# Kernel optimization log

Hardware: AMD Instinct MI355X
Metric: run time of the kernel (lower is better)

The kernel has to match this reference:

```python
import jax, jax.numpy as jnp
import numpy as np

EMBED_DIM = 2048
NUM_HEADS = 16
HEAD_DIM = EMBED_DIM // NUM_HEADS
BASE = 10000.0


def rotate_half(x):
    half = x.shape[-1] // 2
    x1, x2 = x[..., :half], x[..., half:]
    return jnp.concatenate([-x2, x1], axis=-1)


def apply_rope(x, base=BASE):
    # x: [B, H, S, Dh]
    S, Dh = x.shape[-2], x.shape[-1]
    inv_freq = 1.0 / (base ** (jnp.arange(0, Dh, 2, dtype=jnp.float32) / Dh))
    t = jnp.arange(S, dtype=jnp.float32)
    freqs = jnp.einsum('i,j->ij', t, inv_freq)          # [S, Dh/2]
    emb = jnp.concatenate([freqs, freqs], axis=-1)      # [S, Dh]
    return x * jnp.cos(emb) + rotate_half(x) * jnp.sin(emb)


def setup_inputs() -> dict:
    key = jax.random.key(0)
    ks = jax.random.split(key, 9)
    B, S, D = 2, 2048, EMBED_DIM
    xavier = lambda k, shape: jax.random.uniform(
        k, shape, jnp.float32, -1.0, 1.0) * float(np.sqrt(6.0 / (shape[0] + shape[1])))
    return {
        'x': jax.random.normal(ks[0], (B, S, D), jnp.float32),
        'q_w': xavier(ks[1], (D, D)),
        'k_w': xavier(ks[2], (D, D)),
        'v_w': xavier(ks[3], (D, D)),
        'q_b': jnp.zeros((D,), jnp.float32),
        'k_b': jnp.zeros((D,), jnp.float32),
        'v_b': jnp.zeros((D,), jnp.float32),
        'out_w': xavier(ks[4], (D, D)),
        'out_b': jnp.zeros((D,), jnp.float32),
    }


def reference(x, q_w, k_w, v_w, q_b, k_b, v_b, out_w, out_b):
    B, S, D = x.shape
    H, Dh = NUM_HEADS, HEAD_DIM
    scaling = Dh ** -0.5
    # F.linear(x, W, b) = x @ W.T + b
    q = (x @ q_w.T + q_b).reshape(B, S, H, Dh).transpose(0, 2, 1, 3)
    k = (x @ k_w.T + k_b).reshape(B, S, H, Dh).transpose(0, 2, 1, 3)
    v = (x @ v_w.T + v_b).reshape(B, S, H, Dh).transpose(0, 2, 1, 3)
    q = apply_rope(q)
    k = apply_rope(k)
    attn = jnp.einsum('bhqd,bhkd->bhqk', q, k) * scaling
    probs = jax.nn.softmax(attn, axis=-1)
    out = jnp.einsum('bhqk,bhkd->bhqd', probs, v)
    out = out.transpose(0, 2, 1, 3).reshape(B, S, D)
    return out @ out_w.T + out_b
```

## Files before the change

### kernel.cpp

```cpp
#include <hip/hip_runtime.h>
#include <stdint.h>

typedef __bf16 bf16;
typedef __bf16 bf16x4 __attribute__((ext_vector_type(4)));
typedef __bf16 bf16x8 __attribute__((ext_vector_type(8)));
typedef float f32x4 __attribute__((ext_vector_type(4)));
typedef float f32x16 __attribute__((ext_vector_type(16)));

#define DM 2048
#define MM 4096
#define MFMA16(a, b, c) __builtin_amdgcn_mfma_f32_16x16x32_bf16(a, b, c, 0, 0, 0)
#define MFMA32(a, b, c) __builtin_amdgcn_mfma_f32_32x32x16_bf16(a, b, c, 0, 0, 0)

__device__ __forceinline__ void gload_lds16(const void* g, void* l) {
  __builtin_amdgcn_global_load_lds((const __attribute__((address_space(1))) uint32_t*)g,
                                   (__attribute__((address_space(3))) uint32_t*)l, 16, 0, 0);
}

__global__ __launch_bounds__(256) void cvt_f32_bf16(
    const float* __restrict__ s0, const float* __restrict__ s1,
    const float* __restrict__ s2, const float* __restrict__ s3,
    const float* __restrict__ s4,
    bf16* __restrict__ d0, bf16* __restrict__ d1, bf16* __restrict__ d2,
    bf16* __restrict__ d3, bf16* __restrict__ d4)
{
  const size_t i4 = (size_t)(blockIdx.x * 256 + threadIdx.x) * 4;
  const float* s; bf16* d; size_t off;
  if      (i4 <  8388608u) { s = s0; d = d0; off = i4;             }
  else if (i4 < 12582912u) { s = s1; d = d1; off = i4 -  8388608u; }
  else if (i4 < 16777216u) { s = s2; d = d2; off = i4 - 12582912u; }
  else if (i4 < 20971520u) { s = s3; d = d3; off = i4 - 16777216u; }
  else                     { s = s4; d = d4; off = i4 - 20971520u; }
  const float4 v = *(const float4*)(s + off);
  bf16x4 o = { (bf16)v.x, (bf16)v.y, (bf16)v.z, (bf16)v.w };
  *(bf16x4*)(d + off) = o;
}

__global__ __launch_bounds__(256, 2) void gemm_qkv_fused(
    const bf16* __restrict__ A,
    const bf16* __restrict__ Wq, const bf16* __restrict__ Wk, const bf16* __restrict__ Wv,
    const float* __restrict__ qb, const float* __restrict__ kb, const float* __restrict__ vb,
    bf16* __restrict__ Cq, bf16* __restrict__ Ck, bf16* __restrict__ Cv)
{
  __shared__ __align__(16) bf16 smem[32768];
  bf16* As = smem;
  bf16* Ws = smem + 8192;

  const int id = blockIdx.x;
  const int xcd = id & 7, jj = id >> 3;
  const int n0 = (xcd * 2 + (jj >> 5)) * 128;
  const int m0 = (jj & 31) * 128;

  const int t = threadIdx.x;
  const int wave = t >> 6, lane = t & 63;
  const int quad = lane >> 4, c16 = lane & 15;
  const int wr = wave >> 1, wc = wave & 1;

  f32x4 acc[3][4][4] = {};

  const int srow = t >> 3;
  const int scol = ((t & 7) ^ (srow & 7)) * 8;
  const bf16* gA  = A  + (size_t)(m0 + srow) * DM + scol;
  const bf16* gW0 = Wq + (size_t)(n0 + srow) * DM + scol;
  const bf16* gW1 = Wk + (size_t)(n0 + srow) * DM + scol;
  const bf16* gW2 = Wv + (size_t)(n0 + srow) * DM + scol;

  for (int k0 = 0; k0 < DM; k0 += 64) {
#pragma unroll
    for (int rr = 0; rr < 4; ++rr) {
      const size_t go = (size_t)(rr * 32) * DM;
      const int lo = (rr * 256 + wave * 64) * 8;
      gload_lds16(gA  + go, As + lo);
      gload_lds16(gW0 + go, Ws + lo);
      gload_lds16(gW1 + go, Ws + 8192 + lo);
      gload_lds16(gW2 + go, Ws + 16384 + lo);
    }
    gA += 64; gW0 += 64; gW1 += 64; gW2 += 64;
    __syncthreads();

#pragma unroll
    for (int ks = 0; ks < 2; ++ks) {
      bf16x8 af[4];
#pragma unroll
      for (int i = 0; i < 4; ++i) {
        const int row = wr * 64 + i * 16 + c16;
        const int gi = (ks * 4 + quad) ^ (row & 7);
        af[i] = *(const bf16x8*)&As[row * 64 + gi * 8];
      }
#pragma unroll
      for (int z = 0; z < 3; ++z) {
        bf16x8 bfr[4];
#pragma unroll
        for (int jx = 0; jx < 4; ++jx) {
          const int row = wc * 64 + jx * 16 + c16;
          const int gi = (ks * 4 + quad) ^ (row & 7);
          bfr[jx] = *(const bf16x8*)&Ws[z * 8192 + row * 64 + gi * 8];
        }
#pragma unroll
        for (int i = 0; i < 4; ++i)
#pragma unroll
          for (int jx = 0; jx < 4; ++jx)
            acc[z][i][jx] = MFMA16(af[i], bfr[jx], acc[z][i][jx]);
      }
    }
    __syncthreads();
  }

  const int h = n0 >> 7;
#pragma unroll
  for (int jx = 0; jx < 4; ++jx) {
    const int d = wc * 64 + jx * 16 + c16;
    const float bv = vb[n0 + d];
#pragma unroll
    for (int i = 0; i < 4; ++i) {
      const int row = m0 + wr * 64 + i * 16 + quad * 4;
      const int b = row >> 11, s = row & 2047;
      bf16x4 o;
#pragma unroll
      for (int r = 0; r < 4; ++r) o[r] = (bf16)(acc[2][i][jx][r] + bv);
      *(bf16x4*)&Cv[((size_t)((b * 16 + h) * 128 + d)) * 2048 + s] = o;
    }
  }

  bf16* Tl = smem;
#pragma unroll
  for (int z = 0; z < 2; ++z) {
    __syncthreads();
#pragma unroll
    for (int jx = 0; jx < 4; ++jx) {
      const int col = wc * 64 + jx * 16 + c16;
      const float bv = (z == 0 ? qb : kb)[n0 + col];
#pragma unroll
      for (int i = 0; i < 4; ++i) {
        const int row = wr * 64 + i * 16 + quad * 4;
#pragma unroll
        for (int r = 0; r < 4; ++r)
          Tl[(row + r) * 136 + col] = (bf16)(acc[z][i][jx][r] + bv);
      }
    }
    __syncthreads();
    bf16* C = (z == 0) ? Cq : Ck;
    const float scale = (z == 0) ? 0.08838834764831845f * 1.4426950408889634f : 1.0f;
#pragma unroll
    for (int rr = 0; rr < 4; ++rr) {
      const int row = rr * 32 + (t >> 3);
      const int d0 = (t & 7) * 8;
      const int s = (m0 + row) & 2047;
      bf16x8 xa = *(const bf16x8*)&Tl[row * 136 + d0];
      bf16x8 xb = *(const bf16x8*)&Tl[row * 136 + d0 + 64];
      bf16x8 o1, o2;
#pragma unroll
      for (int j = 0; j < 8; ++j) {
        const float inv_freq = __expf((float)(d0 + j) * -0.14391156514261228f);
        float sn, cs;
        __sincosf((float)s * inv_freq, &sn, &cs);
        const float a = (float)xa[j], bb = (float)xb[j];
        o1[j] = (bf16)((a * cs - bb * sn) * scale);
        o2[j] = (bf16)((bb * cs + a * sn) * scale);
      }
      *(bf16x8*)&C[(size_t)(m0 + row) * DM + n0 + d0]      = o1;
      *(bf16x8*)&C[(size_t)(m0 + row) * DM + n0 + d0 + 64] = o2;
    }
  }
}

__global__ __launch_bounds__(256, 2) void gemm_bias_f32(
    const bf16* __restrict__ A, const bf16* __restrict__ W,
    const float* __restrict__ bias, float* __restrict__ C)
{
  __shared__ __align__(16) bf16 As[8192];
  __shared__ __align__(16) bf16 Bs[8192];
  const int id = blockIdx.x;
  const int xcd = id & 7, jj = id >> 3;
  const int n0 = (xcd * 2 + (jj >> 5)) * 128;
  const int m0 = (jj & 31) * 128;

  const int t = threadIdx.x;
  const int wave = t >> 6, lane = t & 63;
  const int quad = lane >> 4, c16 = lane & 15;
  const int wr = wave >> 1, wc = wave & 1;

  f32x4 acc[4][4] = {};
  const int srow = t >> 3;
  const int scol = ((t & 7) ^ (srow & 7)) * 8;
  const bf16* gA = A + (size_t)(m0 + srow) * DM + scol;
  const bf16* gB = W + (size_t)(n0 + srow) * DM + scol;

  for (int k0 = 0; k0 < DM; k0 += 64) {
#pragma unroll
    for (int rr = 0; rr < 4; ++rr) {
      const size_t go = (size_t)(rr * 32) * DM;
      const int lo = (rr * 256 + wave * 64) * 8;
      gload_lds16(gA + go, As + lo);
      gload_lds16(gB + go, Bs + lo);
    }
    gA += 64; gB += 64;
    __syncthreads();

#pragma unroll
    for (int ks = 0; ks < 2; ++ks) {
      bf16x8 af[4], bfr[4];
#pragma unroll
      for (int i = 0; i < 4; ++i) {
        const int row = wr * 64 + i * 16 + c16;
        const int gi = (ks * 4 + quad) ^ (row & 7);
        af[i] = *(const bf16x8*)&As[row * 64 + gi * 8];
      }
#pragma unroll
      for (int jx = 0; jx < 4; ++jx) {
        const int row = wc * 64 + jx * 16 + c16;
        const int gi = (ks * 4 + quad) ^ (row & 7);
        bfr[jx] = *(const bf16x8*)&Bs[row * 64 + gi * 8];
      }
#pragma unroll
      for (int i = 0; i < 4; ++i)
#pragma unroll
        for (int jx = 0; jx < 4; ++jx)
          acc[i][jx] = MFMA16(af[i], bfr[jx], acc[i][jx]);
    }
    __syncthreads();
  }

#pragma unroll
  for (int jx = 0; jx < 4; ++jx) {
    const int col = n0 + wc * 64 + jx * 16 + c16;
    const float bv = bias[col];
#pragma unroll
    for (int i = 0; i < 4; ++i) {
      const int row = m0 + wr * 64 + i * 16 + quad * 4;
#pragma unroll
      for (int r = 0; r < 4; ++r)
        C[(size_t)(row + r) * DM + col] = acc[i][jx][r] + bv;
    }
  }
}

__global__ __launch_bounds__(256, 2) void attn(
    const bf16* __restrict__ Q, const bf16* __restrict__ K,
    const bf16* __restrict__ Vt, bf16* __restrict__ O)
{
  __shared__ __align__(16) bf16 Ks[2][64][128];
  __shared__ __align__(16) bf16 Vs[2][128][64];
  const int t = threadIdx.x;
  const int wave = t >> 6, lane = t & 63;
  const int r31 = lane & 31, h = lane >> 5;
  const int id = blockIdx.x;
  const int xcd = id & 7, jj = id >> 3;
  const int bh = xcd * 4 + (jj >> 4);
  const int q0 = (jj & 15) * 128;
  const int b = bh >> 4, hd = bh & 15;

  bf16x8 qf[8];
  {
    const bf16* qrow = Q + (size_t)(b * 2048 + q0 + wave * 32 + r31) * 2048
                         + (size_t)hd * 128 + h * 8;
#pragma unroll
    for (int ks = 0; ks < 8; ++ks) qf[ks] = *(const bf16x8*)(qrow + ks * 16);
  }

  float l_i = 0.f;
  f32x16 o_acc[4] = {};

  const bf16* Kg = K + (size_t)(b * 2048) * 2048 + (size_t)hd * 128;
  const bf16* Vg = Vt + (size_t)bh * 128 * 2048;

  auto stage = [&](int kt0, int nb) {
#pragma unroll
    for (int rr = 0; rr < 4; ++rr) {
      const int G = rr * 256 + t;
      const int key = G >> 4, gl = G & 15;
      gload_lds16(Kg + (size_t)(kt0 + key) * 2048 + ((gl ^ (key & 7)) * 8),
                  (bf16*)Ks[nb] + (rr * 256 + wave * 64) * 8);
    }
#pragma unroll
    for (int rr = 0; rr < 4; ++rr) {
      const int G = rr * 256 + t;
      const int d = G >> 3, gl = G & 7;
      gload_lds16(Vg + (size_t)d * 2048 + kt0 + ((gl ^ (d & 7)) * 8),
                  (bf16*)Vs[nb] + (rr * 256 + wave * 64) * 8);
    }
  };

  stage(0, 0);
  __syncthreads();

#pragma unroll 2
  for (int kt = 0; kt < 32; ++kt) {
    const int cb = kt & 1;
    if (kt < 31) stage((kt + 1) * 64, cb ^ 1);

#pragma unroll
    for (int rb = 0; rb < 2; ++rb) {
      f32x16 st = {};
#pragma unroll
      for (int ks = 0; ks < 8; ++ks) {
        const int key = rb * 32 + r31;
        const int g = (2 * ks + h) ^ (key & 7);
        bf16x8 kf = *(const bf16x8*)&Ks[cb][key][g * 8];
        st = MFMA32(kf, qf[ks], st);
      }

      float p[16];
#pragma unroll
      for (int r = 0; r < 16; ++r) { p[r] = exp2f(st[r]); l_i += p[r]; }

      uint32_t pka[4], pkb[4];
#pragma unroll
      for (int pp = 0; pp < 4; ++pp) {
        asm("v_cvt_pk_bf16_f32 %0, %1, %2"
            : "=v"(pka[pp]) : "v"(p[4 * pp + 0]), "v"(p[4 * pp + 1]));
        asm("v_cvt_pk_bf16_f32 %0, %1, %2"
            : "=v"(pkb[pp]) : "v"(p[4 * pp + 2]), "v"(p[4 * pp + 3]));
      }

#pragma unroll
      for (int c = 0; c < 2; ++c) {
        uint32_t a0 = pka[2 * c], a1 = pka[2 * c + 1];
        uint32_t b0 = pkb[2 * c], b1 = pkb[2 * c + 1];
        asm("v_permlane32_swap_b32 %0, %1" : "+v"(a0), "+v"(a1));
        asm("v_permlane32_swap_b32 %0, %1" : "+v"(b0), "+v"(b1));
        union { uint32_t u[4]; bf16x8 v; } pf;
        pf.u[0] = a0; pf.u[1] = b0; pf.u[2] = a1; pf.u[3] = b1;
        const int kap = rb * 2 + c;
#pragma unroll
        for (int db = 0; db < 4; ++db) {
          const int d = db * 32 + r31;
          const int g = (2 * kap + h) ^ (d & 7);
          bf16x8 vf = *(const bf16x8*)&Vs[cb][d][g * 8];
          o_acc[db] = MFMA32(vf, pf.v, o_acc[db]);
        }
      }
    }
    __syncthreads();
  }

  l_i += __shfl_xor(l_i, 32, 64);
  const float invl = 1.0f / l_i;
  const int q = q0 + wave * 32 + r31;
  bf16* orow = O + (size_t)(b * 2048 + q) * 2048 + (size_t)hd * 128;
#pragma unroll
  for (int db = 0; db < 4; ++db)
#pragma unroll
    for (int pp = 0; pp < 4; ++pp) {
      const int d0 = db * 32 + 8 * pp + 4 * h;
      bf16x4 o;
#pragma unroll
      for (int r = 0; r < 4; ++r) o[r] = (bf16)(o_acc[db][4 * pp + r] * invl);
      *(bf16x4*)(orow + d0) = o;
    }
}

extern "C" void kernel_launch(void* const* d_in, const int* in_sizes, int n_in,
                              void* d_out, int out_size, void* d_ws, size_t ws_size,
                              hipStream_t stream)
{
  (void)in_sizes; (void)n_in; (void)out_size; (void)ws_size;
  const float* x   = (const float*)d_in[0];
  const float* q_w = (const float*)d_in[1];
  const float* k_w = (const float*)d_in[2];
  const float* v_w = (const float*)d_in[3];
  const float* q_b = (const float*)d_in[4];
  const float* k_b = (const float*)d_in[5];
  const float* v_b = (const float*)d_in[6];
  const float* o_w = (const float*)d_in[7];
  const float* o_b = (const float*)d_in[8];

  const size_t NELEM = (size_t)MM * DM;
  const size_t WELEM = (size_t)DM * DM;
  bf16* Xb  = (bf16*)d_ws;
  bf16* Wq  = Xb + NELEM;
  bf16* Wk  = Wq + WELEM;
  bf16* Wv  = Wk + WELEM;
  bf16* Wo  = Wv + WELEM;
  bf16* Q   = Wo + WELEM;
  bf16* Kb  = Q  + NELEM;
  bf16* Vt  = Kb + NELEM;
  bf16* attnO = Xb;

  cvt_f32_bf16<<<24576, 256, 0, stream>>>(x, q_w, k_w, v_w, o_w, Xb, Wq, Wk, Wv, Wo);

  gemm_qkv_fused<<<512, 256, 0, stream>>>(Xb, Wq, Wk, Wv, q_b, k_b, v_b, Q, Kb, Vt);
  attn<<<512, 256, 0, stream>>>(Q, Kb, Vt, attnO);
  gemm_bias_f32<<<512, 256, 0, stream>>>(attnO, Wo, o_b, (float*)d_out);
}
```

Before: 364.4 us.

## Double-buffer LDS tiles in QKV and output GEMMs with BK=32 prefetch

Both GEMM kernels change from a single-buffered BK=64 loop, which loaded and then synced, to a double-buffered BK=32 loop that prefetches the next K tile into the other LDS buffer while computing on the current one. The LDS layout packs two rows of 32 bf16 per 64-element line with a new XOR swizzle, and read indices are precomputed. The output GEMM's launch bound also rises to 3 blocks per CU. The aim is to hide global-to-LDS load latency, at the cost of twice as many barriers and smaller per-iteration MFMA work.

Result: slower. 387.8 us (+6.4%).

```diff
diff --git a/kernel.cpp b/kernel.cpp
--- a/kernel.cpp
+++ b/kernel.cpp
@@ -43,8 +43,6 @@
     bf16* __restrict__ Cq, bf16* __restrict__ Ck, bf16* __restrict__ Cv)
 {
   __shared__ __align__(16) bf16 smem[32768];
-  bf16* As = smem;
-  bf16* Ws = smem + 8192;
 
   const int id = blockIdx.x;
   const int xcd = id & 7, jj = id >> 3;
@@ -58,50 +56,58 @@
 
   f32x4 acc[3][4][4] = {};
 
-  const int srow = t >> 3;
-  const int scol = ((t & 7) ^ (srow & 7)) * 8;
-  const bf16* gA  = A  + (size_t)(m0 + srow) * DM + scol;
-  const bf16* gW0 = Wq + (size_t)(n0 + srow) * DM + scol;
-  const bf16* gW1 = Wk + (size_t)(n0 + srow) * DM + scol;
-  const bf16* gW2 = Wv + (size_t)(n0 + srow) * DM + scol;
-
-  for (int k0 = 0; k0 < DM; k0 += 64) {
-#pragma unroll
-    for (int rr = 0; rr < 4; ++rr) {
-      const size_t go = (size_t)(rr * 32) * DM;
-      const int lo = (rr * 256 + wave * 64) * 8;
-      gload_lds16(gA  + go, As + lo);
-      gload_lds16(gW0 + go, Ws + lo);
-      gload_lds16(gW1 + go, Ws + 8192 + lo);
-      gload_lds16(gW2 + go, Ws + 16384 + lo);
-    }
-    gA += 64; gW0 += 64; gW1 += 64; gW2 += 64;
-    __syncthreads();
-
-#pragma unroll
-    for (int ks = 0; ks < 2; ++ks) {
-      bf16x8 af[4];
-#pragma unroll
-      for (int i = 0; i < 4; ++i) {
-        const int row = wr * 64 + i * 16 + c16;
-        const int gi = (ks * 4 + quad) ^ (row & 7);
-        af[i] = *(const bf16x8*)&As[row * 64 + gi * 8];
-      }
-#pragma unroll
-      for (int z = 0; z < 3; ++z) {
-        bf16x8 bfr[4];
-#pragma unroll
-        for (int jx = 0; jx < 4; ++jx) {
-          const int row = wc * 64 + jx * 16 + c16;
-          const int gi = (ks * 4 + quad) ^ (row & 7);
-          bfr[jx] = *(const bf16x8*)&Ws[z * 8192 + row * 64 + gi * 8];
-        }
-#pragma unroll
-        for (int i = 0; i < 4; ++i)
-#pragma unroll
-          for (int jx = 0; jx < 4; ++jx)
-            acc[z][i][jx] = MFMA16(af[i], bfr[jx], acc[z][i][jx]);
-      }
+  size_t aRow[2], wRow[2]; int ldsOff[2];
+#pragma unroll
+  for (int rr = 0; rr < 2; ++rr) {
+    const int g = rr * 256 + t;
+    const int r = g >> 3, s = g & 7;
+    const int sp = s ^ (r & 7);
+    const int m = 2 * r + (sp >> 2), k8 = sp & 3;
+    aRow[rr] = (size_t)(m0 + m) * DM + k8 * 8;
+    wRow[rr] = (size_t)(n0 + m) * DM + k8 * 8;
+    ldsOff[rr] = (rr * 256 + wave * 64) * 8;
+  }
+  int aIdx[4], bIdx[4];
+#pragma unroll
+  for (int i = 0; i < 4; ++i) {
+    const int ma = wr * 64 + i * 16 + c16;
+    aIdx[i] = (ma >> 1) * 64 + (((((ma & 1) << 2) | quad)) ^ ((ma >> 1) & 7)) * 8;
+    const int mb = wc * 64 + i * 16 + c16;
+    bIdx[i] = (mb >> 1) * 64 + (((((mb & 1) << 2) | quad)) ^ ((mb >> 1) & 7)) * 8;
+  }
+
+  auto stage = [&](int k0, int nb) {
+#pragma unroll
+    for (int rr = 0; rr < 2; ++rr) {
+      gload_lds16(A  + aRow[rr] + k0, smem + nb * 4096 + ldsOff[rr]);
+      gload_lds16(Wq + wRow[rr] + k0, smem + 8192 + (0 + nb) * 4096 + ldsOff[rr]);
+      gload_lds16(Wk + wRow[rr] + k0, smem + 8192 + (2 + nb) * 4096 + ldsOff[rr]);
+      gload_lds16(Wv + wRow[rr] + k0, smem + 8192 + (4 + nb) * 4096 + ldsOff[rr]);
+    }
+  };
+
+  stage(0, 0);
+  __syncthreads();
+
+#pragma unroll 2
+  for (int kt = 0; kt < 64; ++kt) {
+    const int cb = kt & 1;
+    if (kt < 63) stage((kt + 1) * 32, cb ^ 1);
+
+    bf16x8 af[4];
+#pragma unroll
+    for (int i = 0; i < 4; ++i) af[i] = *(const bf16x8*)&smem[cb * 4096 + aIdx[i]];
+#pragma unroll
+    for (int z = 0; z < 3; ++z) {
+      const bf16* Wb = smem + 8192 + (z * 2 + cb) * 4096;
+      bf16x8 bfr[4];
+#pragma unroll
+      for (int jx = 0; jx < 4; ++jx) bfr[jx] = *(const bf16x8*)&Wb[bIdx[jx]];
+#pragma unroll
+      for (int i = 0; i < 4; ++i)
+#pragma unroll
+        for (int jx = 0; jx < 4; ++jx)
+          acc[z][i][jx] = MFMA16(af[i], bfr[jx], acc[z][i][jx]);
     }
     __syncthreads();
   }
@@ -164,12 +170,11 @@
   }
 }
 
-__global__ __launch_bounds__(256, 2) void gemm_bias_f32(
+__global__ __launch_bounds__(256, 3) void gemm_bias_f32(
     const bf16* __restrict__ A, const bf16* __restrict__ W,
     const float* __restrict__ bias, float* __restrict__ C)
 {
-  __shared__ __align__(16) bf16 As[8192];
-  __shared__ __align__(16) bf16 Bs[8192];
+  __shared__ __align__(16) bf16 smem[16384];
   const int id = blockIdx.x;
   const int xcd = id & 7, jj = id >> 3;
   const int n0 = (xcd * 2 + (jj >> 5)) * 128;
@@ -181,43 +186,54 @@
   const int wr = wave >> 1, wc = wave & 1;
 
   f32x4 acc[4][4] = {};
-  const int srow = t >> 3;
-  const int scol = ((t & 7) ^ (srow & 7)) * 8;
-  const bf16* gA = A + (size_t)(m0 + srow) * DM + scol;
-  const bf16* gB = W + (size_t)(n0 + srow) * DM + scol;
-
-  for (int k0 = 0; k0 < DM; k0 += 64) {
-#pragma unroll
-    for (int rr = 0; rr < 4; ++rr) {
-      const size_t go = (size_t)(rr * 32) * DM;
-      const int lo = (rr * 256 + wave * 64) * 8;
-      gload_lds16(gA + go, As + lo);
-      gload_lds16(gB + go, Bs + lo);
-    }
-    gA += 64; gB += 64;
-    __syncthreads();
-
-#pragma unroll
-    for (int ks = 0; ks < 2; ++ks) {
-      bf16x8 af[4], bfr[4];
-#pragma unroll
-      for (int i = 0; i < 4; ++i) {
-        const int row = wr * 64 + i * 16 + c16;
-        const int gi = (ks * 4 + quad) ^ (row & 7);
-        af[i] = *(const bf16x8*)&As[row * 64 + gi * 8];
-      }
-#pragma unroll
-      for (int jx = 0; jx < 4; ++jx) {
-        const int row = wc * 64 + jx * 16 + c16;
-        const int gi = (ks * 4 + quad) ^ (row & 7);
-        bfr[jx] = *(const bf16x8*)&Bs[row * 64 + gi * 8];
-      }
-#pragma unroll
-      for (int i = 0; i < 4; ++i)
-#pragma unroll
-        for (int jx = 0; jx < 4; ++jx)
-          acc[i][jx] = MFMA16(af[i], bfr[jx], acc[i][jx]);
-    }
+
+  size_t aRow[2], bRow[2]; int ldsOff[2];
+#pragma unroll
+  for (int rr = 0; rr < 2; ++rr) {
+    const int g = rr * 256 + t;
+    const int r = g >> 3, s = g & 7;
+    const int sp = s ^ (r & 7);
+    const int m = 2 * r + (sp >> 2), k8 = sp & 3;
+    aRow[rr] = (size_t)(m0 + m) * DM + k8 * 8;
+    bRow[rr] = (size_t)(n0 + m) * DM + k8 * 8;
+    ldsOff[rr] = (rr * 256 + wave * 64) * 8;
+  }
+  int aIdx[4], bIdx[4];
+#pragma unroll
+  for (int i = 0; i < 4; ++i) {
+    const int ma = wr * 64 + i * 16 + c16;
+    aIdx[i] = (ma >> 1) * 64 + (((((ma & 1) << 2) | quad)) ^ ((ma >> 1) & 7)) * 8;
+    const int mb = wc * 64 + i * 16 + c16;
+    bIdx[i] = (mb >> 1) * 64 + (((((mb & 1) << 2) | quad)) ^ ((mb >> 1) & 7)) * 8;
+  }
+
+  auto stage = [&](int k0, int nb) {
+#pragma unroll
+    for (int rr = 0; rr < 2; ++rr) {
+      gload_lds16(A + aRow[rr] + k0, smem + nb * 4096 + ldsOff[rr]);
+      gload_lds16(W + bRow[rr] + k0, smem + 8192 + nb * 4096 + ldsOff[rr]);
+    }
+  };
+
+  stage(0, 0);
+  __syncthreads();
+
+#pragma unroll 2
+  for (int kt = 0; kt < 64; ++kt) {
+    const int cb = kt & 1;
+    if (kt < 63) stage((kt + 1) * 32, cb ^ 1);
+
+    bf16x8 af[4], bfr[4];
+#pragma unroll
+    for (int i = 0; i < 4; ++i) {
+      af[i]  = *(const bf16x8*)&smem[cb * 4096 + aIdx[i]];
+      bfr[i] = *(const bf16x8*)&smem[8192 + cb * 4096 + bIdx[i]];
+    }
+#pragma unroll
+    for (int i = 0; i < 4; ++i)
+#pragma unroll
+      for (int jx = 0; jx < 4; ++jx)
+        acc[i][jx] = MFMA16(af[i], bfr[jx], acc[i][jx]);
     __syncthreads();
   }
 
```

## Double query rows per attention block to reuse K/V tiles; tighten barrier waits

Applied to the files above, without the earlier changes.

Each attention wave now processes two 32-row query slices (256 queries per block), so every K/V fragment read from LDS feeds two MFMAs. The grid is halved to 256 blocks and launch bounds drop to one block per SM to make room for the extra registers. The __syncthreads calls are replaced by explicit vmcnt waits plus s_barrier, so the prefetch of the next tile overlaps compute. The cost is higher register pressure, lower occupancy and only 256 blocks, which may underfill the 256 CUs.

Result: slower. 378.1 us (+3.8%).

```diff
diff --git a/kernel.cpp b/kernel.cpp
--- a/kernel.cpp
+++ b/kernel.cpp
@@ -11,6 +11,9 @@
 #define MM 4096
 #define MFMA16(a, b, c) __builtin_amdgcn_mfma_f32_16x16x32_bf16(a, b, c, 0, 0, 0)
 #define MFMA32(a, b, c) __builtin_amdgcn_mfma_f32_32x32x16_bf16(a, b, c, 0, 0, 0)
+
+#define WAITV_BAR(N) asm volatile("s_waitcnt vmcnt(" #N ")\n\ts_barrier" ::: "memory")
+#define BAR()        asm volatile("s_barrier" ::: "memory")
 
 __device__ __forceinline__ void gload_lds16(const void* g, void* l) {
   __builtin_amdgcn_global_load_lds((const __attribute__((address_space(1))) uint32_t*)g,
@@ -235,7 +238,7 @@
   }
 }
 
-__global__ __launch_bounds__(256, 2) void attn(
+__global__ __launch_bounds__(256, 1) void attn(
     const bf16* __restrict__ Q, const bf16* __restrict__ K,
     const bf16* __restrict__ Vt, bf16* __restrict__ O)
 {
@@ -246,20 +249,21 @@
   const int r31 = lane & 31, h = lane >> 5;
   const int id = blockIdx.x;
   const int xcd = id & 7, jj = id >> 3;
-  const int bh = xcd * 4 + (jj >> 4);
-  const int q0 = (jj & 15) * 128;
+  const int bh = xcd * 4 + (jj >> 3);
+  const int q0 = (jj & 7) * 256;
   const int b = bh >> 4, hd = bh & 15;
 
-  bf16x8 qf[8];
-  {
-    const bf16* qrow = Q + (size_t)(b * 2048 + q0 + wave * 32 + r31) * 2048
+  bf16x8 qf[2][8];
+#pragma unroll
+  for (int qs = 0; qs < 2; ++qs) {
+    const bf16* qrow = Q + (size_t)(b * 2048 + q0 + wave * 64 + qs * 32 + r31) * 2048
                          + (size_t)hd * 128 + h * 8;
 #pragma unroll
-    for (int ks = 0; ks < 8; ++ks) qf[ks] = *(const bf16x8*)(qrow + ks * 16);
-  }
-
-  float l_i = 0.f;
-  f32x16 o_acc[4] = {};
+    for (int ks = 0; ks < 8; ++ks) qf[qs][ks] = *(const bf16x8*)(qrow + ks * 16);
+  }
+
+  float l_i[2] = {0.f, 0.f};
+  f32x16 o_acc[2][4] = {};
 
   const bf16* Kg = K + (size_t)(b * 2048) * 2048 + (size_t)hd * 128;
   const bf16* Vg = Vt + (size_t)bh * 128 * 2048;
@@ -282,72 +286,89 @@
   };
 
   stage(0, 0);
-  __syncthreads();
-
-#pragma unroll 2
+
   for (int kt = 0; kt < 32; ++kt) {
     const int cb = kt & 1;
-    if (kt < 31) stage((kt + 1) * 64, cb ^ 1);
+    if (kt < 31) {
+      stage((kt + 1) * 64, cb ^ 1);
+      WAITV_BAR(8);
+    } else {
+      WAITV_BAR(0);
+    }
 
 #pragma unroll
     for (int rb = 0; rb < 2; ++rb) {
-      f32x16 st = {};
+      f32x16 st[2] = {};
 #pragma unroll
       for (int ks = 0; ks < 8; ++ks) {
         const int key = rb * 32 + r31;
         const int g = (2 * ks + h) ^ (key & 7);
         bf16x8 kf = *(const bf16x8*)&Ks[cb][key][g * 8];
-        st = MFMA32(kf, qf[ks], st);
-      }
-
-      float p[16];
-#pragma unroll
-      for (int r = 0; r < 16; ++r) { p[r] = exp2f(st[r]); l_i += p[r]; }
-
-      uint32_t pka[4], pkb[4];
-#pragma unroll
-      for (int pp = 0; pp < 4; ++pp) {
-        asm("v_cvt_pk_bf16_f32 %0, %1, %2"
-            : "=v"(pka[pp]) : "v"(p[4 * pp + 0]), "v"(p[4 * pp + 1]));
-        asm("v_cvt_pk_bf16_f32 %0, %1, %2"
-            : "=v"(pkb[pp]) : "v"(p[4 * pp + 2]), "v"(p[4 * pp + 3]));
+        st[0] = MFMA32(kf, qf[0][ks], st[0]);
+        st[1] = MFMA32(kf, qf[1][ks], st[1]);
+      }
+
+      uint32_t pf[2][2][4];
+#pragma unroll
+      for (int qs = 0; qs < 2; ++qs) {
+        float p[16];
+#pragma unroll
+        for (int r = 0; r < 16; ++r) { p[r] = exp2f(st[qs][r]); l_i[qs] += p[r]; }
+        uint32_t pka[4], pkb[4];
+#pragma unroll
+        for (int pp = 0; pp < 4; ++pp) {
+          asm("v_cvt_pk_bf16_f32 %0, %1, %2"
+              : "=v"(pka[pp]) : "v"(p[4 * pp + 0]), "v"(p[4 * pp + 1]));
+          asm("v_cvt_pk_bf16_f32 %0, %1, %2"
+              : "=v"(pkb[pp]) : "v"(p[4 * pp + 2]), "v"(p[4 * pp + 3]));
+        }
+#pragma unroll
+        for (int c = 0; c < 2; ++c) {
+          uint32_t a0 = pka[2 * c], a1 = pka[2 * c + 1];
+          uint32_t b0 = pkb[2 * c], b1 = pkb[2 * c + 1];
+          asm("v_permlane32_swap_b32 %0, %1" : "+v"(a0), "+v"(a1));
+          asm("v_permlane32_swap_b32 %0, %1" : "+v"(b0), "+v"(b1));
+          pf[qs][c][0] = a0; pf[qs][c][1] = b0; pf[qs][c][2] = a1; pf[qs][c][3] = b1;
+        }
       }
 
 #pragma unroll
       for (int c = 0; c < 2; ++c) {
-        uint32_t a0 = pka[2 * c], a1 = pka[2 * c + 1];
-        uint32_t b0 = pkb[2 * c], b1 = pkb[2 * c + 1];
-        asm("v_permlane32_swap_b32 %0, %1" : "+v"(a0), "+v"(a1));
-        asm("v_permlane32_swap_b32 %0, %1" : "+v"(b0), "+v"(b1));
-        union { uint32_t u[4]; bf16x8 v; } pf;
-        pf.u[0] = a0; pf.u[1] = b0; pf.u[2] = a1; pf.u[3] = b1;
         const int kap = rb * 2 + c;
+        union { uint32_t u[4]; bf16x8 v; } p0, p1;
+#pragma unroll
+        for (int w = 0; w < 4; ++w) { p0.u[w] = pf[0][c][w]; p1.u[w] = pf[1][c][w]; }
 #pragma unroll
         for (int db = 0; db < 4; ++db) {
           const int d = db * 32 + r31;
           const int g = (2 * kap + h) ^ (d & 7);
           bf16x8 vf = *(const bf16x8*)&Vs[cb][d][g * 8];
-          o_acc[db] = MFMA32(vf, pf.v, o_acc[db]);
+          o_acc[0][db] = MFMA32(vf, p0.v, o_acc[0][db]);
+          o_acc[1][db] = MFMA32(vf, p1.v, o_acc[1][db]);
         }
       }
     }
-    __syncthreads();
-  }
-
-  l_i += __shfl_xor(l_i, 32, 64);
-  const float invl = 1.0f / l_i;
-  const int q = q0 + wave * 32 + r31;
-  bf16* orow = O + (size_t)(b * 2048 + q) * 2048 + (size_t)hd * 128;
-#pragma unroll
-  for (int db = 0; db < 4; ++db)
-#pragma unroll
-    for (int pp = 0; pp < 4; ++pp) {
-      const int d0 = db * 32 + 8 * pp + 4 * h;
-      bf16x4 o;
-#pragma unroll
-      for (int r = 0; r < 4; ++r) o[r] = (bf16)(o_acc[db][4 * pp + r] * invl);
-      *(bf16x4*)(orow + d0) = o;
-    }
+    BAR();
+  }
+
+#pragma unroll
+  for (int qs = 0; qs < 2; ++qs) {
+    float l = l_i[qs];
+    l += __shfl_xor(l, 32, 64);
+    const float invl = 1.0f / l;
+    const int q = q0 + wave * 64 + qs * 32 + r31;
+    bf16* orow = O + (size_t)(b * 2048 + q) * 2048 + (size_t)hd * 128;
+#pragma unroll
+    for (int db = 0; db < 4; ++db)
+#pragma unroll
+      for (int pp = 0; pp < 4; ++pp) {
+        const int d0 = db * 32 + 8 * pp + 4 * h;
+        bf16x4 o;
+#pragma unroll
+        for (int r = 0; r < 4; ++r) o[r] = (bf16)(o_acc[qs][db][4 * pp + r] * invl);
+        *(bf16x4*)(orow + d0) = o;
+      }
+  }
 }
 
 extern "C" void kernel_launch(void* const* d_in, const int* in_sizes, int n_in,
@@ -380,6 +401,6 @@
   cvt_f32_bf16<<<24576, 256, 0, stream>>>(x, q_w, k_w, v_w, o_w, Xb, Wq, Wk, Wv, Wo);
 
   gemm_qkv_fused<<<512, 256, 0, stream>>>(Xb, Wq, Wk, Wv, q_b, k_b, v_b, Q, Kb, Vt);
-  attn<<<512, 256, 0, stream>>>(Q, Kb, Vt, attnO);
+  attn<<<256, 256, 0, stream>>>(Q, Kb, Vt, attnO);
   gemm_bias_f32<<<512, 256, 0, stream>>>(attnO, Wo, o_b, (float*)d_out);
 }
```

## Load V fragments straight to registers and restructure K staging barriers

Applied to the files above, without the earlier changes.

The attention kernel no longer stages V through LDS. Each lane loads its V MFMA fragments for the tile directly from global memory into registers, while K keeps its double-buffered LDS staging. The synchronisation is now hand-written with s_waitcnt vmcnt and s_barrier, and both QK score blocks are computed before the softmax and PV work, so the barrier sits earlier. This frees LDS and removes the V LDS round trip, but every wave now fetches the same V tile from global memory and needs many more registers for the vv array.

Result: slower. 425.0 us (+16.6%).

```diff
diff --git a/kernel.cpp b/kernel.cpp
--- a/kernel.cpp
+++ b/kernel.cpp
@@ -11,6 +11,9 @@
 #define MM 4096
 #define MFMA16(a, b, c) __builtin_amdgcn_mfma_f32_16x16x32_bf16(a, b, c, 0, 0, 0)
 #define MFMA32(a, b, c) __builtin_amdgcn_mfma_f32_32x32x16_bf16(a, b, c, 0, 0, 0)
+
+#define WAITV_BAR(N) asm volatile("s_waitcnt vmcnt(" #N ")\n\ts_barrier" ::: "memory")
+#define BAR()        asm volatile("s_barrier" ::: "memory")
 
 __device__ __forceinline__ void gload_lds16(const void* g, void* l) {
   __builtin_amdgcn_global_load_lds((const __attribute__((address_space(1))) uint32_t*)g,
@@ -240,7 +243,6 @@
     const bf16* __restrict__ Vt, bf16* __restrict__ O)
 {
   __shared__ __align__(16) bf16 Ks[2][64][128];
-  __shared__ __align__(16) bf16 Vs[2][128][64];
   const int t = threadIdx.x;
   const int wave = t >> 6, lane = t & 63;
   const int r31 = lane & 31, h = lane >> 5;
@@ -262,9 +264,9 @@
   f32x16 o_acc[4] = {};
 
   const bf16* Kg = K + (size_t)(b * 2048) * 2048 + (size_t)hd * 128;
-  const bf16* Vg = Vt + (size_t)bh * 128 * 2048;
-
-  auto stage = [&](int kt0, int nb) {
+  const bf16* Vlane = Vt + (size_t)bh * 128 * 2048 + (size_t)r31 * 2048 + h * 8;
+
+  auto stageK = [&](int kt0, int nb) {
 #pragma unroll
     for (int rr = 0; rr < 4; ++rr) {
       const int G = rr * 256 + t;
@@ -272,34 +274,44 @@
       gload_lds16(Kg + (size_t)(kt0 + key) * 2048 + ((gl ^ (key & 7)) * 8),
                   (bf16*)Ks[nb] + (rr * 256 + wave * 64) * 8);
     }
-#pragma unroll
-    for (int rr = 0; rr < 4; ++rr) {
-      const int G = rr * 256 + t;
-      const int d = G >> 3, gl = G & 7;
-      gload_lds16(Vg + (size_t)d * 2048 + kt0 + ((gl ^ (d & 7)) * 8),
-                  (bf16*)Vs[nb] + (rr * 256 + wave * 64) * 8);
-    }
   };
 
-  stage(0, 0);
-  __syncthreads();
-
-#pragma unroll 2
+  stageK(0, 0);
+
   for (int kt = 0; kt < 32; ++kt) {
     const int cb = kt & 1;
-    if (kt < 31) stage((kt + 1) * 64, cb ^ 1);
+    const int kt0 = kt * 64;
+
+    bf16x8 vv[16];
+#pragma unroll
+    for (int kap = 0; kap < 4; ++kap)
+#pragma unroll
+      for (int db = 0; db < 4; ++db)
+        vv[kap * 4 + db] =
+            *(const bf16x8*)(Vlane + (size_t)db * 65536 + kt0 + kap * 16);
+
+    if (kt < 31) {
+      stageK(kt0 + 64, cb ^ 1);
+      WAITV_BAR(20);
+    } else {
+      WAITV_BAR(16);
+    }
+
+    f32x16 st0 = {}, st1 = {};
+#pragma unroll
+    for (int ks = 0; ks < 8; ++ks) {
+      const int g = (2 * ks + h) ^ (r31 & 7);
+      bf16x8 kf0 = *(const bf16x8*)&Ks[cb][r31][g * 8];
+      bf16x8 kf1 = *(const bf16x8*)&Ks[cb][32 + r31][g * 8];
+      st0 = MFMA32(kf0, qf[ks], st0);
+      st1 = MFMA32(kf1, qf[ks], st1);
+    }
+
+    BAR();
 
 #pragma unroll
     for (int rb = 0; rb < 2; ++rb) {
-      f32x16 st = {};
-#pragma unroll
-      for (int ks = 0; ks < 8; ++ks) {
-        const int key = rb * 32 + r31;
-        const int g = (2 * ks + h) ^ (key & 7);
-        bf16x8 kf = *(const bf16x8*)&Ks[cb][key][g * 8];
-        st = MFMA32(kf, qf[ks], st);
-      }
-
+      const f32x16& st = (rb == 0) ? st0 : st1;
       float p[16];
 #pragma unroll
       for (int r = 0; r < 16; ++r) { p[r] = exp2f(st[r]); l_i += p[r]; }
@@ -312,7 +324,6 @@
         asm("v_cvt_pk_bf16_f32 %0, %1, %2"
             : "=v"(pkb[pp]) : "v"(p[4 * pp + 2]), "v"(p[4 * pp + 3]));
       }
-
 #pragma unroll
       for (int c = 0; c < 2; ++c) {
         uint32_t a0 = pka[2 * c], a1 = pka[2 * c + 1];
@@ -323,15 +334,10 @@
         pf.u[0] = a0; pf.u[1] = b0; pf.u[2] = a1; pf.u[3] = b1;
         const int kap = rb * 2 + c;
 #pragma unroll
-        for (int db = 0; db < 4; ++db) {
-          const int d = db * 32 + r31;
-          const int g = (2 * kap + h) ^ (d & 7);
-          bf16x8 vf = *(const bf16x8*)&Vs[cb][d][g * 8];
-          o_acc[db] = MFMA32(vf, pf.v, o_acc[db]);
-        }
-      }
-    }
-    __syncthreads();
+        for (int db = 0; db < 4; ++db)
+          o_acc[db] = MFMA32(vv[kap * 4 + db], pf.v, o_acc[db]);
+      }
+    }
   }
 
   l_i += __shfl_xor(l_i, 32, 64);
```
